# Performance work log

Hardware: AMD Instinct MI355X
Metric: run time of the kernel (lower is better)

## Reference

```python
import jax, jax.numpy as jnp
import numpy as np

DIM = 128
HEADS = 8
HD = DIM // HEADS          # head_dim = 16
WS = 4                     # window_size
T = WS ** 3                # tokens per window = 64
G = 8                      # num_global_tokens
RATIO = 0.1                # global_attention_ratio
SCALE = HD ** -0.5


def setup_inputs() -> dict:
    key = jax.random.key(0)
    ks = jax.random.split(key, 8)
    B, D, H, W = 4, 32, 32, 32
    init = lambda k, shape: (jax.random.normal(k, shape, jnp.float32) * 0.02)
    return {
        "features": jax.random.normal(ks[0], (B, D, H, W, DIM), jnp.float32),
        "Wqkv": init(ks[1], (DIM, 3 * DIM)),
        "bqkv": jnp.zeros((3 * DIM,), jnp.float32),
        "Wout": init(ks[2], (DIM, DIM)),
        "bout": jnp.zeros((DIM,), jnp.float32),
        "Wqg": init(ks[3], (DIM, DIM)),
        "bqg": jnp.zeros((DIM,), jnp.float32),
        "Wkvg": init(ks[4], (DIM, 2 * DIM)),
        "bkvg": jnp.zeros((2 * DIM,), jnp.float32),
        "Woutg": init(ks[5], (DIM, DIM)),
        "boutg": jnp.zeros((DIM,), jnp.float32),
        "g_tokens": init(ks[6], (1, G, DIM)),
    }


def reference(features, Wqkv, bqkv, Wout, bout, Wqg, bqg, Wkvg, bkvg, Woutg, boutg, g_tokens):
    B, D, H, W, C = features.shape
    nd, nh, nw = D // WS, H // WS, W // WS  # assumes dims divisible by WS (pad path unused)

    # ---- window partition: (B, D, H, W, C) -> (B*num_windows, T, C) ----
    x = features.reshape(B, nd, WS, nh, WS, nw, WS, C)
    x = x.transpose(0, 1, 3, 5, 2, 4, 6, 7)
    windows = x.reshape(-1, T, C)

    # ---- local attention within each window ----
    qkv = windows @ Wqkv + bqkv                                # (N, T, 3C)
    qkv = qkv.reshape(-1, T, 3, HEADS, HD).transpose(2, 0, 3, 1, 4)
    q, k, v = qkv[0], qkv[1], qkv[2]                           # (N, heads, T, HD)
    attn = jax.nn.softmax(jnp.einsum('nhqd,nhkd->nhqk', q, k) * SCALE, axis=-1)
    out = jnp.einsum('nhqk,nhkd->nhqd', attn, v)
    out = out.transpose(0, 2, 1, 3).reshape(-1, T, C)
    out = out @ Wout + bout

    # ---- window unpartition ----
    out = out.reshape(B, nd, nh, nw, WS, WS, WS, C)
    out = out.transpose(0, 1, 4, 2, 5, 3, 6, 7)
    local_out = out.reshape(B, D, H, W, C)

    # ---- global token cross-attention ----
    x_flat = features.reshape(B, -1, C)                        # (B, S, C), S = D*H*W
    qg = (x_flat @ Wqg + bqg).reshape(B, -1, HEADS, HD).transpose(0, 2, 1, 3)  # (B, h, S, HD)
    gt = jnp.broadcast_to(g_tokens, (B, G, C))
    kv = (gt @ Wkvg + bkvg).reshape(B, G, 2, HEADS, HD).transpose(2, 0, 3, 1, 4)
    kg, vg = kv[0], kv[1]                                      # (B, h, G, HD)
    ag = jax.nn.softmax(jnp.einsum('bhqd,bhkd->bhqk', qg, kg) * SCALE, axis=-1)
    go = jnp.einsum('bhqk,bhkd->bhqd', ag, vg)
    go = go.transpose(0, 2, 1, 3).reshape(B, -1, C)
    go = (go @ Woutg + boutg).reshape(B, D, H, W, C)

    return local_out + RATIO * go
```

## Files before the change

kernel.cpp:

```cpp
#include <hip/hip_runtime.h>
#include <hip/hip_bf16.h>

typedef __bf16 bf16x8 __attribute__((ext_vector_type(8)));
typedef __bf16 bf16x4 __attribute__((ext_vector_type(4)));
typedef float  f32x4  __attribute__((ext_vector_type(4)));

#define WS_B1T   0
#define WS_B2T   131072
#define WS_BIAS1 196608
#define WS_BIAS2 198656
#define WS_KVG   199168

__global__ __launch_bounds__(256) void wattn_prep(
    const float* __restrict__ Wqkv, const float* __restrict__ bqkv,
    const float* __restrict__ Wout, const float* __restrict__ bout,
    const float* __restrict__ Wqg,  const float* __restrict__ bqg,
    const float* __restrict__ Wkvg, const float* __restrict__ bkvg,
    const float* __restrict__ Woutg,const float* __restrict__ boutg,
    const float* __restrict__ gtok, unsigned char* __restrict__ ws)
{
    const int blk = blockIdx.x, tid = threadIdx.x;
    __bf16* B1t = (__bf16*)(ws + WS_B1T);
    __bf16* B2t = (__bf16*)(ws + WS_B2T);
    float* bias1 = (float*)(ws + WS_BIAS1);
    float* bias2 = (float*)(ws + WS_BIAS2);
    float* kvg   = (float*)(ws + WS_KVG);

    if (blk < 32) {
        #pragma unroll
        for (int j = 0; j < 8; ++j) {
            const int i = blk*2048 + j*256 + tid;
            const int k = i >> 9, n = i & 511;
            const float w = (n < 384) ? Wqkv[k*384 + n] : Wqg[k*128 + (n - 384)];
            B1t[n*128 + k] = (__bf16)w;
        }
    } else if (blk < 48) {
        #pragma unroll
        for (int j = 0; j < 8; ++j) {
            const int i = (blk - 32)*2048 + j*256 + tid;
            const int k = i >> 8, n = i & 255;
            const float w = (n < 128) ? Wout[k*128 + n] : 0.1f * Woutg[k*128 + (n - 128)];
            B2t[n*128 + k] = (__bf16)w;
        }
    } else if (blk < 56) {
        const int g = blk - 48;
        const int j = tid;
        float acc = bkvg[j];
        #pragma unroll 8
        for (int c = 0; c < 128; ++c) acc += gtok[g*128 + c] * Wkvg[c*256 + j];
        kvg[(j >> 7)*1024 + ((j >> 4) & 7)*128 + (j & 15)*8 + g] = acc;
    } else {
        for (int i = tid; i < 512; i += 256) bias1[i] = (i < 384) ? bqkv[i] : bqg[i - 384];
        for (int i = tid; i < 128; i += 256) bias2[i] = bout[i] + 0.1f * boutg[i];
    }
}

__global__ __launch_bounds__(512, 4) void wattn_main(
    const float* __restrict__ feat,
    const unsigned char* __restrict__ ws,
    float* __restrict__ out)
{
    __shared__ __align__(16) unsigned char lds[65536];
    const int tid  = threadIdx.x;
    const int h    = tid >> 6;
    const int lane = tid & 63;
    const int rg   = lane >> 4;
    const int cl   = lane & 15;

    const int blk = blockIdx.x;
    const int b   = blk >> 9;
    const int rem = blk & 511;
    const int base_row = b*32768 + (rem >> 6)*4096 + ((rem >> 3) & 7)*128 + (rem & 7)*4;

    const uint4 z4i = {0u, 0u, 0u, 0u};
    const bf16x8 zfrag = __builtin_bit_cast(bf16x8, z4i);
    const f32x4 z4 = {0.f, 0.f, 0.f, 0.f};

    unsigned char* Qs = lds + 16384 + h*2048;
    unsigned char* Ks = lds + 32768 + h*2048;
    unsigned char* Vs = lds + 49152 + h*2048;

    {
        const int row = tid >> 3, j = tid & 7;
        const int grow = base_row + (row >> 4)*1024 + ((row >> 2) & 3)*32 + (row & 3);
        const float* src = feat + grow*128;
        #pragma unroll
        for (int hh = 0; hh < 2; ++hh) {
            const int col = hh*64 + j*8;
            float4 a = *(const float4*)(src + col);
            float4 c = *(const float4*)(src + col + 4);
            bf16x8 v;
            v[0] = (__bf16)a.x; v[1] = (__bf16)a.y; v[2] = (__bf16)a.z; v[3] = (__bf16)a.w;
            v[4] = (__bf16)c.x; v[5] = (__bf16)c.y; v[6] = (__bf16)c.z; v[7] = (__bf16)c.w;
            *(bf16x8*)(lds + ((row*256 + col*2) ^ ((row & 7) << 4))) = v;
        }
    }
    __syncthreads();

    f32x4 acc[4][4];
    {
        const __bf16* B1t = (const __bf16*)(ws + WS_B1T);
        const float* bias1 = (const float*)(ws + WS_BIAS1);
        const int ntile[4] = {h, 8 + h, 16 + h, 24 + h};
        #pragma unroll
        for (int i = 0; i < 4; ++i) {
            const float bv = bias1[ntile[i]*16 + cl];
            f32x4 t = {bv, bv, bv, bv};
            #pragma unroll
            for (int mt = 0; mt < 4; ++mt) acc[mt][i] = t;
        }
        #pragma unroll
        for (int ks = 0; ks < 4; ++ks) {
            bf16x8 afr[4];
            #pragma unroll
            for (int mt = 0; mt < 4; ++mt) {
                const int row = mt*16 + cl, col = ks*32 + rg*8;
                afr[mt] = *(const bf16x8*)(lds + ((row*256 + col*2) ^ ((row & 7) << 4)));
            }
            #pragma unroll
            for (int i = 0; i < 4; ++i) {
                bf16x8 bfr = *(const bf16x8*)(B1t + ntile[i]*16*128 + cl*128 + ks*32 + rg*8);
                #pragma unroll
                for (int mt = 0; mt < 4; ++mt)
                    acc[mt][i] = __builtin_amdgcn_mfma_f32_16x16x32_bf16(afr[mt], bfr, acc[mt][i], 0, 0, 0);
            }
        }
    }
    #pragma unroll
    for (int mt = 0; mt < 4; ++mt) {
        #pragma unroll
        for (int r = 0; r < 4; ++r) {
            const int t = mt*16 + rg*4 + r;
            const int off = (t*32 + cl*2) ^ ((t & 4) << 2);
            *(__bf16*)(Qs + off) = (__bf16)acc[mt][0][r];
            *(__bf16*)(Ks + off) = (__bf16)acc[mt][1][r];
        }
        bf16x4 pv;
        #pragma unroll
        for (int r = 0; r < 4; ++r) pv[r] = (__bf16)acc[mt][2][r];
        const int t0 = mt*16 + rg*4;
        *(bf16x4*)(Vs + ((cl*128 + t0*2) ^ ((cl & 7) << 4))) = pv;
    }
    __syncthreads();

    f32x4 o[4] = {z4, z4, z4, z4};
    float rinv[4];
    bf16x8 kf[4];
    #pragma unroll
    for (int kt = 0; kt < 4; ++kt) {
        if (rg < 2) {
            const int row = kt*16 + cl;
            kf[kt] = *(const bf16x8*)(Ks + ((row*32 + rg*16) ^ ((cl & 4) << 2)));
        } else kf[kt] = zfrag;
    }
    #pragma unroll
    for (int half = 0; half < 2; ++half) {
        const int q0t = half*2;
        bf16x8 qf[2];
        #pragma unroll
        for (int i = 0; i < 2; ++i) {
            if (rg < 2) {
                const int row = (q0t + i)*16 + cl;
                qf[i] = *(const bf16x8*)(Qs + ((row*32 + rg*16) ^ ((cl & 4) << 2)));
            } else qf[i] = zfrag;
        }
        f32x4 s[4][2];
        #pragma unroll
        for (int kt = 0; kt < 4; ++kt)
            #pragma unroll
            for (int i = 0; i < 2; ++i)
                s[kt][i] = __builtin_amdgcn_mfma_f32_16x16x32_bf16(kf[kt], qf[i], z4, 0, 0, 0);
        #pragma unroll
        for (int i = 0; i < 2; ++i) {
            float m = -1e30f;
            #pragma unroll
            for (int kt = 0; kt < 4; ++kt)
                m = fmaxf(m, fmaxf(fmaxf(s[kt][i][0], s[kt][i][1]), fmaxf(s[kt][i][2], s[kt][i][3])));
            m = fmaxf(m, __shfl_xor(m, 16));
            m = fmaxf(m, __shfl_xor(m, 32));
            float sm = 0.f;
            #pragma unroll
            for (int kt = 0; kt < 4; ++kt)
                #pragma unroll
                for (int r = 0; r < 4; ++r) {
                    const float e = __expf((s[kt][i][r] - m) * 0.25f);
                    s[kt][i][r] = e;
                    sm += e;
                }
            sm += __shfl_xor(sm, 16);
            sm += __shfl_xor(sm, 32);
            rinv[q0t + i] = 1.0f / sm;
        }
        unsigned char* Pslot = half ? Qs : Ks;
        #pragma unroll
        for (int sl = 0; sl < 2; ++sl) {
            #pragma unroll
            for (int i = 0; i < 2; ++i) {
                const int q = (q0t + i)*16 + cl;
                unsigned char* Pb = Pslot + (q & 31)*64;
                #pragma unroll
                for (int kk = 0; kk < 2; ++kk) {
                    const int kt = sl*2 + kk;
                    bf16x4 pp;
                    #pragma unroll
                    for (int r = 0; r < 4; ++r) pp[r] = (__bf16)s[kt][i][r];
                    *(bf16x4*)(Pb + ((kk*32 + rg*8) ^ ((q & 3) << 4))) = pp;
                }
            }
            const bf16x8 vf = *(const bf16x8*)(Vs + ((cl*128 + sl*64 + rg*16) ^ ((cl & 7) << 4)));
            #pragma unroll
            for (int i = 0; i < 2; ++i) {
                const int q = (q0t + i)*16 + cl;
                const bf16x8 pf = *(const bf16x8*)(Pslot + (q & 31)*64 + ((rg*16) ^ ((q & 3) << 4)));
                o[q0t + i] = __builtin_amdgcn_mfma_f32_16x16x32_bf16(vf, pf, o[q0t + i], 0, 0, 0);
            }
        }
    }
    #pragma unroll
    for (int qt = 0; qt < 4; ++qt) {
        const int t = qt*16 + cl;
        bf16x4 ov;
        #pragma unroll
        for (int r = 0; r < 4; ++r) ov[r] = (__bf16)(o[qt][r] * rinv[qt]);
        *(bf16x4*)(lds + ((t*256 + h*32 + rg*8) ^ ((t & 7) << 4))) = ov;
    }
    #pragma unroll
    for (int mt = 0; mt < 4; ++mt) {
        bf16x4 pq;
        #pragma unroll
        for (int r = 0; r < 4; ++r) pq[r] = (__bf16)acc[mt][3][r];
        const int t0 = mt*16 + rg*4;
        *(bf16x4*)(Qs + ((cl*128 + t0*2) ^ ((cl & 7) << 4))) = pq;
    }

    float got[16];
    {
        float qgv[16];
        #pragma unroll
        for (int d = 0; d < 16; ++d)
            qgv[d] = (float)*(const __bf16*)(Qs + ((d*128 + lane*2) ^ ((d & 7) << 4)));
        const float* kgT = (const float*)(ws + WS_KVG) + h*128;
        const float* vgT = kgT + 1024;
        float lg[8] = {0.f,0.f,0.f,0.f,0.f,0.f,0.f,0.f};
        #pragma unroll
        for (int d = 0; d < 16; ++d) {
            const float4 k0 = *(const float4*)(kgT + d*8);
            const float4 k1 = *(const float4*)(kgT + d*8 + 4);
            const float qv = qgv[d];
            lg[0] += qv*k0.x; lg[1] += qv*k0.y; lg[2] += qv*k0.z; lg[3] += qv*k0.w;
            lg[4] += qv*k1.x; lg[5] += qv*k1.y; lg[6] += qv*k1.z; lg[7] += qv*k1.w;
        }
        float m = fmaxf(fmaxf(fmaxf(lg[0], lg[1]), fmaxf(lg[2], lg[3])),
                        fmaxf(fmaxf(lg[4], lg[5]), fmaxf(lg[6], lg[7])));
        float sm = 0.f;
        float p[8];
        #pragma unroll
        for (int g = 0; g < 8; ++g) { p[g] = __expf((lg[g] - m) * 0.25f); sm += p[g]; }
        const float rs = 1.0f / sm;
        #pragma unroll
        for (int g = 0; g < 8; ++g) p[g] *= rs;
        #pragma unroll
        for (int d = 0; d < 16; ++d) {
            const float4 v0 = *(const float4*)(vgT + d*8);
            const float4 v1 = *(const float4*)(vgT + d*8 + 4);
            got[d] = p[0]*v0.x + p[1]*v0.y + p[2]*v0.z + p[3]*v0.w
                   + p[4]*v1.x + p[5]*v1.y + p[6]*v1.z + p[7]*v1.w;
        }
    }
    __syncthreads();

    {
        bf16x8 g0, g1;
        #pragma unroll
        for (int j = 0; j < 8; ++j) { g0[j] = (__bf16)got[j]; g1[j] = (__bf16)got[8 + j]; }
        *(bf16x8*)(lds + 32768 + ((lane*256 + h*32)      ^ ((lane & 7) << 4))) = g0;
        *(bf16x8*)(lds + 32768 + ((lane*256 + h*32 + 16) ^ ((lane & 7) << 4))) = g1;
    }
    __syncthreads();

    {
        const __bf16* B2t = (const __bf16*)(ws + WS_B2T);
        const float* bias2 = (const float*)(ws + WS_BIAS2);
        f32x4 y[4];
        const float4 bv = *(const float4*)(bias2 + h*16 + rg*4);
        #pragma unroll
        for (int tt = 0; tt < 4; ++tt) { f32x4 t = {bv.x, bv.y, bv.z, bv.w}; y[tt] = t; }
        #pragma unroll
        for (int ks = 0; ks < 4; ++ks) {
            const bf16x8 aW = *(const bf16x8*)(B2t + (h*16 + cl)*128 + ks*32 + rg*8);
            const bf16x8 aG = *(const bf16x8*)(B2t + (128 + h*16 + cl)*128 + ks*32 + rg*8);
            #pragma unroll
            for (int tt = 0; tt < 4; ++tt) {
                const int t = tt*16 + cl;
                const int off = (t*256 + ks*64 + rg*16) ^ ((t & 7) << 4);
                const bf16x8 bO = *(const bf16x8*)(lds + off);
                const bf16x8 bG = *(const bf16x8*)(lds + 32768 + off);
                y[tt] = __builtin_amdgcn_mfma_f32_16x16x32_bf16(aW, bO, y[tt], 0, 0, 0);
                y[tt] = __builtin_amdgcn_mfma_f32_16x16x32_bf16(aG, bG, y[tt], 0, 0, 0);
            }
        }
        #pragma unroll
        for (int tt = 0; tt < 4; ++tt) {
            const int grow = base_row + tt*1024 + (cl >> 2)*32 + (cl & 3);
            *(f32x4*)(out + grow*128 + h*16 + rg*4) = y[tt];
        }
    }
}

extern "C" void kernel_launch(void* const* d_in, const int* in_sizes, int n_in,
                              void* d_out, int out_size, void* d_ws, size_t ws_size,
                              hipStream_t stream) {
    (void)in_sizes; (void)n_in; (void)out_size; (void)ws_size;
    const float* feat  = (const float*)d_in[0];
    const float* Wqkv  = (const float*)d_in[1];
    const float* bqkv  = (const float*)d_in[2];
    const float* Wout  = (const float*)d_in[3];
    const float* bout  = (const float*)d_in[4];
    const float* Wqg   = (const float*)d_in[5];
    const float* bqg   = (const float*)d_in[6];
    const float* Wkvg  = (const float*)d_in[7];
    const float* bkvg  = (const float*)d_in[8];
    const float* Woutg = (const float*)d_in[9];
    const float* boutg = (const float*)d_in[10];
    const float* gtok  = (const float*)d_in[11];
    unsigned char* ws  = (unsigned char*)d_ws;

    wattn_prep<<<dim3(57), dim3(256), 0, stream>>>(
        Wqkv, bqkv, Wout, bout, Wqg, bqg, Wkvg, bkvg, Woutg, boutg, gtok, ws);
    wattn_main<<<dim3(2048), dim3(512), 0, stream>>>(feat, ws, (float*)d_out);
}
```

Before: 233.8 us.

## Halve LDS footprint by aliasing Q/K/V buffers and retile output projection

Shrinks shared memory from 64KB to 32KB per block by reusing the input-tile region for Q and P, and a single per-head buffer for K, then V, then the global query. Launch bounds are raised to allow more resident blocks per CU. Q fragments are now loaded into registers up front, and the attention output write is moved after the barrier, so it can overwrite the reused region safely. The output projection is retiled as 2x2 MFMA tiles per wave to reuse fragments across tiles. The risk is register pressure from the tighter launch bound and the extra Q registers, plus subtle ordering hazards in the buffer reuse.

```diff
diff --git a/kernel.cpp b/kernel.cpp
--- a/kernel.cpp
+++ b/kernel.cpp
@@ -55,12 +55,12 @@
     }
 }
 
-__global__ __launch_bounds__(512, 4) void wattn_main(
+__global__ __launch_bounds__(512, 8) void wattn_main(
     const float* __restrict__ feat,
     const unsigned char* __restrict__ ws,
     float* __restrict__ out)
 {
-    __shared__ __align__(16) unsigned char lds[65536];
+    __shared__ __align__(16) unsigned char lds[32768];
     const int tid  = threadIdx.x;
     const int h    = tid >> 6;
     const int lane = tid & 63;
@@ -76,9 +76,8 @@
     const bf16x8 zfrag = __builtin_bit_cast(bf16x8, z4i);
     const f32x4 z4 = {0.f, 0.f, 0.f, 0.f};
 
-    unsigned char* Qs = lds + 16384 + h*2048;
-    unsigned char* Ks = lds + 32768 + h*2048;
-    unsigned char* Vs = lds + 49152 + h*2048;
+    unsigned char* Xh  = lds + h*2048;
+    unsigned char* KVh = lds + 16384 + h*2048;
 
     {
         const int row = tid >> 3, j = tid & 7;
@@ -127,49 +126,57 @@
         }
     }
     #pragma unroll
-    for (int mt = 0; mt < 4; ++mt) {
+    for (int mt = 0; mt < 4; ++mt)
         #pragma unroll
         for (int r = 0; r < 4; ++r) {
             const int t = mt*16 + rg*4 + r;
-            const int off = (t*32 + cl*2) ^ ((t & 4) << 2);
-            *(__bf16*)(Qs + off) = (__bf16)acc[mt][0][r];
-            *(__bf16*)(Ks + off) = (__bf16)acc[mt][1][r];
-        }
-        bf16x4 pv;
-        #pragma unroll
-        for (int r = 0; r < 4; ++r) pv[r] = (__bf16)acc[mt][2][r];
-        const int t0 = mt*16 + rg*4;
-        *(bf16x4*)(Vs + ((cl*128 + t0*2) ^ ((cl & 7) << 4))) = pv;
-    }
+            *(__bf16*)(KVh + ((t*32 + cl*2) ^ ((t & 4) << 2))) = (__bf16)acc[mt][1][r];
+        }
     __syncthreads();
 
-    f32x4 o[4] = {z4, z4, z4, z4};
-    float rinv[4];
+    #pragma unroll
+    for (int mt = 0; mt < 4; ++mt)
+        #pragma unroll
+        for (int r = 0; r < 4; ++r) {
+            const int t = mt*16 + rg*4 + r;
+            *(__bf16*)(Xh + ((t*32 + cl*2) ^ ((t & 4) << 2))) = (__bf16)acc[mt][0][r];
+        }
     bf16x8 kf[4];
     #pragma unroll
     for (int kt = 0; kt < 4; ++kt) {
         if (rg < 2) {
             const int row = kt*16 + cl;
-            kf[kt] = *(const bf16x8*)(Ks + ((row*32 + rg*16) ^ ((cl & 4) << 2)));
+            kf[kt] = *(const bf16x8*)(KVh + ((row*32 + rg*16) ^ ((cl & 4) << 2)));
         } else kf[kt] = zfrag;
     }
+    #pragma unroll
+    for (int mt = 0; mt < 4; ++mt) {
+        bf16x4 pv;
+        #pragma unroll
+        for (int r = 0; r < 4; ++r) pv[r] = (__bf16)acc[mt][2][r];
+        const int t0 = mt*16 + rg*4;
+        *(bf16x4*)(KVh + ((cl*128 + t0*2) ^ ((cl & 7) << 4))) = pv;
+    }
+    bf16x8 qf[4];
+    #pragma unroll
+    for (int qt = 0; qt < 4; ++qt) {
+        if (rg < 2) {
+            const int row = qt*16 + cl;
+            qf[qt] = *(const bf16x8*)(Xh + ((row*32 + rg*16) ^ ((cl & 4) << 2)));
+        } else qf[qt] = zfrag;
+    }
+
+    f32x4 o[4] = {z4, z4, z4, z4};
+    float rinv[4];
     #pragma unroll
     for (int half = 0; half < 2; ++half) {
         const int q0t = half*2;
-        bf16x8 qf[2];
-        #pragma unroll
-        for (int i = 0; i < 2; ++i) {
-            if (rg < 2) {
-                const int row = (q0t + i)*16 + cl;
-                qf[i] = *(const bf16x8*)(Qs + ((row*32 + rg*16) ^ ((cl & 4) << 2)));
-            } else qf[i] = zfrag;
-        }
         f32x4 s[4][2];
         #pragma unroll
         for (int kt = 0; kt < 4; ++kt)
             #pragma unroll
             for (int i = 0; i < 2; ++i)
-                s[kt][i] = __builtin_amdgcn_mfma_f32_16x16x32_bf16(kf[kt], qf[i], z4, 0, 0, 0);
+                s[kt][i] = __builtin_amdgcn_mfma_f32_16x16x32_bf16(kf[kt], qf[q0t + i], z4, 0, 0, 0);
         #pragma unroll
         for (int i = 0; i < 2; ++i) {
             float m = -1e30f;
@@ -191,13 +198,12 @@
             sm += __shfl_xor(sm, 32);
             rinv[q0t + i] = 1.0f / sm;
         }
-        unsigned char* Pslot = half ? Qs : Ks;
         #pragma unroll
         for (int sl = 0; sl < 2; ++sl) {
             #pragma unroll
             for (int i = 0; i < 2; ++i) {
                 const int q = (q0t + i)*16 + cl;
-                unsigned char* Pb = Pslot + (q & 31)*64;
+                unsigned char* Pb = Xh + (q & 31)*64;
                 #pragma unroll
                 for (int kk = 0; kk < 2; ++kk) {
                     const int kt = sl*2 + kk;
@@ -207,22 +213,14 @@
                     *(bf16x4*)(Pb + ((kk*32 + rg*8) ^ ((q & 3) << 4))) = pp;
                 }
             }
-            const bf16x8 vf = *(const bf16x8*)(Vs + ((cl*128 + sl*64 + rg*16) ^ ((cl & 7) << 4)));
+            const bf16x8 vf = *(const bf16x8*)(KVh + ((cl*128 + sl*64 + rg*16) ^ ((cl & 7) << 4)));
             #pragma unroll
             for (int i = 0; i < 2; ++i) {
                 const int q = (q0t + i)*16 + cl;
-                const bf16x8 pf = *(const bf16x8*)(Pslot + (q & 31)*64 + ((rg*16) ^ ((q & 3) << 4)));
+                const bf16x8 pf = *(const bf16x8*)(Xh + (q & 31)*64 + ((rg*16) ^ ((q & 3) << 4)));
                 o[q0t + i] = __builtin_amdgcn_mfma_f32_16x16x32_bf16(vf, pf, o[q0t + i], 0, 0, 0);
             }
         }
-    }
-    #pragma unroll
-    for (int qt = 0; qt < 4; ++qt) {
-        const int t = qt*16 + cl;
-        bf16x4 ov;
-        #pragma unroll
-        for (int r = 0; r < 4; ++r) ov[r] = (__bf16)(o[qt][r] * rinv[qt]);
-        *(bf16x4*)(lds + ((t*256 + h*32 + rg*8) ^ ((t & 7) << 4))) = ov;
     }
     #pragma unroll
     for (int mt = 0; mt < 4; ++mt) {
@@ -230,7 +228,7 @@
         #pragma unroll
         for (int r = 0; r < 4; ++r) pq[r] = (__bf16)acc[mt][3][r];
         const int t0 = mt*16 + rg*4;
-        *(bf16x4*)(Qs + ((cl*128 + t0*2) ^ ((cl & 7) << 4))) = pq;
+        *(bf16x4*)(KVh + ((cl*128 + t0*2) ^ ((cl & 7) << 4))) = pq;
     }
 
     float got[16];
@@ -238,7 +236,7 @@
         float qgv[16];
         #pragma unroll
         for (int d = 0; d < 16; ++d)
-            qgv[d] = (float)*(const __bf16*)(Qs + ((d*128 + lane*2) ^ ((d & 7) << 4)));
+            qgv[d] = (float)*(const __bf16*)(KVh + ((d*128 + lane*2) ^ ((d & 7) << 4)));
         const float* kgT = (const float*)(ws + WS_KVG) + h*128;
         const float* vgT = kgT + 1024;
         float lg[8] = {0.f,0.f,0.f,0.f,0.f,0.f,0.f,0.f};
@@ -269,40 +267,64 @@
     }
     __syncthreads();
 
+    #pragma unroll
+    for (int qt = 0; qt < 4; ++qt) {
+        const int t = qt*16 + cl;
+        bf16x4 ov;
+        #pragma unroll
+        for (int r = 0; r < 4; ++r) ov[r] = (__bf16)(o[qt][r] * rinv[qt]);
+        *(bf16x4*)(lds + ((t*256 + h*32 + rg*8) ^ ((t & 7) << 4))) = ov;
+    }
     {
         bf16x8 g0, g1;
         #pragma unroll
         for (int j = 0; j < 8; ++j) { g0[j] = (__bf16)got[j]; g1[j] = (__bf16)got[8 + j]; }
-        *(bf16x8*)(lds + 32768 + ((lane*256 + h*32)      ^ ((lane & 7) << 4))) = g0;
-        *(bf16x8*)(lds + 32768 + ((lane*256 + h*32 + 16) ^ ((lane & 7) << 4))) = g1;
+        *(bf16x8*)(lds + 16384 + ((lane*256 + h*32)      ^ ((lane & 7) << 4))) = g0;
+        *(bf16x8*)(lds + 16384 + ((lane*256 + h*32 + 16) ^ ((lane & 7) << 4))) = g1;
     }
     __syncthreads();
 
     {
         const __bf16* B2t = (const __bf16*)(ws + WS_B2T);
         const float* bias2 = (const float*)(ws + WS_BIAS2);
-        f32x4 y[4];
-        const float4 bv = *(const float4*)(bias2 + h*16 + rg*4);
-        #pragma unroll
-        for (int tt = 0; tt < 4; ++tt) { f32x4 t = {bv.x, bv.y, bv.z, bv.w}; y[tt] = t; }
+        const int a = h & 3, bb = h >> 2;
+        f32x4 y[2][2];
+        #pragma unroll
+        for (int j = 0; j < 2; ++j) {
+            const float4 bv = *(const float4*)(bias2 + (2*a + j)*16 + rg*4);
+            #pragma unroll
+            for (int i = 0; i < 2; ++i) { f32x4 t = {bv.x, bv.y, bv.z, bv.w}; y[i][j] = t; }
+        }
         #pragma unroll
         for (int ks = 0; ks < 4; ++ks) {
-            const bf16x8 aW = *(const bf16x8*)(B2t + (h*16 + cl)*128 + ks*32 + rg*8);
-            const bf16x8 aG = *(const bf16x8*)(B2t + (128 + h*16 + cl)*128 + ks*32 + rg*8);
-            #pragma unroll
-            for (int tt = 0; tt < 4; ++tt) {
-                const int t = tt*16 + cl;
+            bf16x8 aW[2], aG[2], bO[2], bG[2];
+            #pragma unroll
+            for (int j = 0; j < 2; ++j) {
+                const int n = (2*a + j)*16 + cl;
+                aW[j] = *(const bf16x8*)(B2t + n*128 + ks*32 + rg*8);
+                aG[j] = *(const bf16x8*)(B2t + (128 + n)*128 + ks*32 + rg*8);
+            }
+            #pragma unroll
+            for (int i = 0; i < 2; ++i) {
+                const int t = (2*bb + i)*16 + cl;
                 const int off = (t*256 + ks*64 + rg*16) ^ ((t & 7) << 4);
-                const bf16x8 bO = *(const bf16x8*)(lds + off);
-                const bf16x8 bG = *(const bf16x8*)(lds + 32768 + off);
-                y[tt] = __builtin_amdgcn_mfma_f32_16x16x32_bf16(aW, bO, y[tt], 0, 0, 0);
-                y[tt] = __builtin_amdgcn_mfma_f32_16x16x32_bf16(aG, bG, y[tt], 0, 0, 0);
-            }
-        }
-        #pragma unroll
-        for (int tt = 0; tt < 4; ++tt) {
-            const int grow = base_row + tt*1024 + (cl >> 2)*32 + (cl & 3);
-            *(f32x4*)(out + grow*128 + h*16 + rg*4) = y[tt];
+                bO[i] = *(const bf16x8*)(lds + off);
+                bG[i] = *(const bf16x8*)(lds + 16384 + off);
+            }
+            #pragma unroll
+            for (int i = 0; i < 2; ++i)
+                #pragma unroll
+                for (int j = 0; j < 2; ++j) {
+                    y[i][j] = __builtin_amdgcn_mfma_f32_16x16x32_bf16(aW[j], bO[i], y[i][j], 0, 0, 0);
+                    y[i][j] = __builtin_amdgcn_mfma_f32_16x16x32_bf16(aG[j], bG[i], y[i][j], 0, 0, 0);
+                }
+        }
+        #pragma unroll
+        for (int i = 0; i < 2; ++i) {
+            const int grow = base_row + (2*bb + i)*1024 + (cl >> 2)*32 + (cl & 3);
+            #pragma unroll
+            for (int j = 0; j < 2; ++j)
+                *(f32x4*)(out + grow*128 + (2*a + j)*16 + rg*4) = y[i][j];
         }
     }
 }
```

After: 476.8 us. +103.9%, slower.
